# Optimization experiments

Measured on AMD Instinct MI355X. Metric: run time of the kernel, lower is better.

The kernel has to match this reference:

```python
import jax, jax.numpy as jnp
import numpy as np

B, S, D, H = 64, 128, 1024, 8
DK = D // H  # 128 == S, required by the module's (attn@V)@V quirk
DFF = 2048
EPS = 1e-12


def layernorm(x, w, b):
    u = x.mean(-1, keepdims=True)
    s = ((x - u) ** 2).mean(-1, keepdims=True)
    return w * (x - u) / jnp.sqrt(s + EPS) + b


def setup_inputs() -> dict:
    key = jax.random.key(0)
    ks = jax.random.split(key, 10)
    w = lambda k, shape: jax.random.normal(k, shape, jnp.float32) * 0.02
    return {
        "x": jax.random.normal(ks[0], (B, S, D), jnp.float32),
        "mask": jnp.ones((1, 1, S, S), jnp.int32),
        "Wq": w(ks[1], (D, D)), "bq": jnp.zeros((D,), jnp.float32),
        "Wk": w(ks[2], (D, D)), "bk": jnp.zeros((D,), jnp.float32),
        "Wv": w(ks[3], (D, D)), "bv": jnp.zeros((D,), jnp.float32),
        "Wo": w(ks[4], (D, D)), "bo": jnp.zeros((D,), jnp.float32),
        "ln1_w": jnp.ones((D,), jnp.float32), "ln1_b": jnp.zeros((D,), jnp.float32),
        "W1": w(ks[5], (DFF, D)), "b1": jnp.zeros((DFF,), jnp.float32),
        "W2": w(ks[6], (4 * D, DFF)), "b2": jnp.zeros((4 * D,), jnp.float32),
        "W3": w(ks[7], (D, 4 * D)), "b3": jnp.zeros((D,), jnp.float32),
        "ln2_w": jnp.ones((D,), jnp.float32), "ln2_b": jnp.zeros((D,), jnp.float32),
    }


def reference(x, mask, Wq, bq, Wk, bk, Wv, bv, Wo, bo, ln1_w, ln1_b,
              W1, b1, W2, b2, W3, b3, ln2_w, ln2_b):
    # QKV projections -> [B, H, S, DK]
    Q = (x @ Wq.T + bq).reshape(B, S, H, DK).transpose(0, 2, 1, 3)
    K = (x @ Wk.T + bk).reshape(B, S, H, DK).transpose(0, 2, 1, 3)
    V = (x @ Wv.T + bv).reshape(B, S, H, DK).transpose(0, 2, 1, 3)

    scores = jnp.einsum('bhqd,bhkd->bhqk', Q, K) / jnp.sqrt(jnp.float32(DK))
    scores = jnp.where(mask == 0, jnp.float32(-1e9), scores)
    attn = jax.nn.softmax(scores, axis=-1)  # dropout = identity (eval)
    av = jnp.matmul(attn, V)                 # [B,H,S,DK]
    # Faithful quirk in the source: multiply by V a second time (DK == S).
    ctx = jnp.matmul(av, V)                  # [B,H,S,DK]
    ctx = ctx.transpose(0, 2, 1, 3).reshape(B, S, D)
    attn_out = ctx @ Wo.T + bo

    h = layernorm(x + attn_out, ln1_w, ln1_b)

    f = jax.nn.relu(h @ W1.T + b1)           # [B,S,DFF]
    f = jax.nn.relu(f @ W2.T + b2)           # [B,S,4D]
    f = f @ W3.T + b3                        # [B,S,D]

    return layernorm(h + f, ln2_w, ln2_b)
```

## Files before the change

### kernel.cpp

```cpp
#include <hip/hip_runtime.h>
#include <hip/hip_bf16.h>

using bf16 = __hip_bfloat16;
typedef __attribute__((ext_vector_type(4))) float f32x4;
typedef __attribute__((ext_vector_type(8))) short bf16x8;

__device__ __forceinline__ unsigned short bfbits(float f) {
    bf16 h = __float2bfloat16(f);
    return __builtin_bit_cast(unsigned short, h);
}

__device__ __forceinline__ void g2l16(const void* g, void* l) {
    __builtin_amdgcn_global_load_lds(
        (const __attribute__((address_space(1))) unsigned int*)g,
        (__attribute__((address_space(3))) unsigned int*)l, 16, 0, 0);
}

__global__ void castk(const float* __restrict__ in, bf16* __restrict__ out, int n4) {
    int stride = gridDim.x * blockDim.x;
    for (int i = blockIdx.x * blockDim.x + threadIdx.x; i < n4; i += stride) {
        float4 v = reinterpret_cast<const float4*>(in)[i];
        ushort4 o;
        o.x = bfbits(v.x); o.y = bfbits(v.y); o.z = bfbits(v.z); o.w = bfbits(v.w);
        reinterpret_cast<ushort4*>(out)[i] = o;
    }
}

template<int EPI, int SPLITK>
__global__ __launch_bounds__(512, 2)
void gemm256(const bf16* __restrict__ A, const bf16* __restrict__ Bm,
             int N, int ldk, int kloop,
             const float* __restrict__ bias0, const float* __restrict__ bias1,
             const float* __restrict__ bias2,
             void* __restrict__ outp,
             bf16* __restrict__ q_o, bf16* __restrict__ k_o, bf16* __restrict__ v_o) {
    __shared__ __align__(16) char lds[98304];
    const int tid = threadIdx.x;
    const int lane = tid & 63, wave = tid >> 6;
    const int rlo = lane & 15, g = lane >> 4;
    const int wr = wave >> 2, wc = wave & 3;
    const int nbn = N >> 8;
    const int nwg = gridDim.x;
    int wg = (int)blockIdx.x;
    wg = (wg & 7) * (nwg >> 3) + (wg >> 3);
    int slice = 0;
    if constexpr (SPLITK) {
        int half = nwg >> 1;
        slice = (wg >= half) ? 1 : 0;
        wg -= slice * half;
    }
    const int bm = wg / nbn, bn = wg % nbn;
    const size_t ldb = (size_t)ldk * 2;
    const char* abase = (const char*)A + ((size_t)bm << 8) * ldb + (size_t)slice * kloop * 2;
    const char* bbase = (const char*)Bm + ((size_t)bn << 8) * ldb + (size_t)slice * kloop * 2;

    const int P = tid * 16;
    const int R = P >> 7;
    const int qs = (P & 127) ^ ((R & 7) << 4);
    const size_t goff0 = (size_t)(R * 2 + (qs >> 6)) * ldb + (qs & 63);
    const size_t ghalf = (size_t)128 * ldb;

    const int o_in = (((rlo & 1) << 6) | (g << 4)) ^ (((rlo >> 1) & 7) << 4);
    const int aoff = wr * 8192 + (rlo >> 1) * 128 + o_in;
    const int boff = 16384 + (wc >> 1) * 8192 + (wc & 1) * 4096 + (rlo >> 1) * 128 + o_in;

    const f32x4 fz = {0.f, 0.f, 0.f, 0.f};
    f32x4 acc[8][4];
#pragma unroll
    for (int i = 0; i < 8; ++i)
#pragma unroll
        for (int j = 0; j < 4; ++j) acc[i][j] = fz;

    auto stA = [&](int buf, int h, int kt) {
        g2l16(abase + goff0 + (size_t)h * ghalf + (size_t)kt * 64,
              lds + buf * 32768 + h * 8192 + P);
    };
    auto stB = [&](int buf, int h, int kt) {
        g2l16(bbase + goff0 + (size_t)h * ghalf + (size_t)kt * 64,
              lds + buf * 32768 + 16384 + h * 8192 + P);
    };

    stA(0, 0, 0); stA(0, 1, 0); stB(0, 0, 0); stB(0, 1, 0);
    stA(1, 0, 1); stA(1, 1, 1); stB(1, 0, 1); stB(1, 1, 1);
    asm volatile("s_waitcnt vmcnt(4)" ::: "memory");
    __builtin_amdgcn_s_barrier();
    __builtin_amdgcn_sched_barrier(0);

    const int NT = kloop >> 5;
    for (int kt = 0; kt < NT; ++kt) {
        const char* lb = lds + (kt % 3) * 32768;
        const int nbuf = (kt + 2) % 3;
        const bool pre = (kt + 2) < NT;

        bf16x8 bfr[4], afr[4];
#pragma unroll
        for (int nf = 0; nf < 4; ++nf)
            bfr[nf] = *reinterpret_cast<const bf16x8*>(lb + nf * 1024 + boff);
#pragma unroll
        for (int i = 0; i < 4; ++i)
            afr[i] = *reinterpret_cast<const bf16x8*>(lb + i * 1024 + aoff);
        if (pre) { stA(nbuf, 0, kt + 2); stA(nbuf, 1, kt + 2); }
        asm volatile("s_waitcnt lgkmcnt(0)");
        __builtin_amdgcn_s_setprio(1);
#pragma unroll
        for (int i = 0; i < 4; ++i)
#pragma unroll
            for (int nf = 0; nf < 4; ++nf)
                acc[i][nf] = __builtin_amdgcn_mfma_f32_16x16x32_bf16(afr[i], bfr[nf], acc[i][nf], 0, 0, 0);
        __builtin_amdgcn_s_setprio(0);

#pragma unroll
        for (int i = 0; i < 4; ++i)
            afr[i] = *reinterpret_cast<const bf16x8*>(lb + (4 + i) * 1024 + aoff);
        if (pre) { stB(nbuf, 0, kt + 2); stB(nbuf, 1, kt + 2); }
        asm volatile("s_waitcnt lgkmcnt(0)");
        __builtin_amdgcn_s_setprio(1);
#pragma unroll
        for (int i = 0; i < 4; ++i)
#pragma unroll
            for (int nf = 0; nf < 4; ++nf)
                acc[4 + i][nf] = __builtin_amdgcn_mfma_f32_16x16x32_bf16(afr[i], bfr[nf], acc[4 + i][nf], 0, 0, 0);
        __builtin_amdgcn_s_setprio(0);

        if (pre) {
            asm volatile("s_waitcnt vmcnt(4)" ::: "memory");
        } else if (kt + 1 < NT) {
            asm volatile("s_waitcnt vmcnt(0)" ::: "memory");
        }
        if (kt + 1 < NT) {
            __builtin_amdgcn_s_barrier();
            __builtin_amdgcn_sched_barrier(0);
        }
    }

    const int gm0 = (bm << 8) + wr * 128;
    const int gn0 = (bn << 8) + wc * 64;
#pragma unroll
    for (int mf = 0; mf < 8; ++mf) {
#pragma unroll
        for (int nf = 0; nf < 4; ++nf) {
            const int gnc = gn0 + nf * 16 + rlo;
#pragma unroll
            for (int r = 0; r < 4; ++r) {
                const int gmr = gm0 + mf * 16 + g * 4 + r;
                float val = acc[mf][nf][r];
                if constexpr (EPI == 0) {
                    int t = gnc >> 10;
                    const float* bp = (t == 0) ? bias0 : ((t == 1) ? bias1 : bias2);
                    val += bp[gnc & 1023];
                    bf16* dst = (t == 0) ? q_o : ((t == 1) ? k_o : v_o);
                    int hh = (gnc >> 7) & 7, d = gnc & 127;
                    int bb = gmr >> 7, s = gmr & 127;
                    dst[(((size_t)bb * 8 + hh) * 128 + s) * 128 + d] = __float2bfloat16(val);
                } else if constexpr (EPI == 1) {
                    val = fmaxf(val + bias0[gnc], 0.f);
                    ((bf16*)outp)[(size_t)gmr * N + gnc] = __float2bfloat16(val);
                } else {
                    float* pp = (float*)outp + (size_t)slice * 8388608;
                    pp[(size_t)gmr * N + gnc] = val;
                }
            }
        }
    }
}

template<int EPI>
__global__ __launch_bounds__(256, 2)
void gemm_bt(const bf16* __restrict__ A, const bf16* __restrict__ Bm,
             int M, int N, int K,
             const float* __restrict__ bias0, const float* __restrict__ resid,
             void* __restrict__ outp) {
    (void)M;
    __shared__ __align__(16) char As[8192];
    __shared__ __align__(16) char Bs[8192];
    int tid = threadIdx.x, wave = tid >> 6, lane = tid & 63;
    int nbn = N >> 7;
    int bm = blockIdx.x / nbn, bn = blockIdx.x % nbn;
    int wm = (wave >> 1) << 6, wn = (wave & 1) << 6;
    int rlo = lane & 15, g = lane >> 4;

    const char* abase = (const char*)(A + (size_t)(bm << 7) * K);
    const char* bbase = (const char*)(Bm + (size_t)(bn << 7) * K);

    const f32x4 fzero = {0.f, 0.f, 0.f, 0.f};
    f32x4 acc[4][4];
#pragma unroll
    for (int i = 0; i < 4; ++i)
#pragma unroll
        for (int j = 0; j < 4; ++j) acc[i][j] = fzero;

    int L0 = wave * 2048 + lane * 16;
    size_t ldbyte = (size_t)K * 2;

    for (int k0 = 0; k0 < K; k0 += 32) {
#pragma unroll
        for (int j = 0; j < 2; ++j) {
            int L = L0 + j * 1024;
            int row = L >> 6;
            int cb = (L & 63) ^ (((row >> 1) & 3) << 4);
            g2l16(abase + (size_t)row * ldbyte + (size_t)k0 * 2 + cb, As + wave * 2048 + j * 1024);
            g2l16(bbase + (size_t)row * ldbyte + (size_t)k0 * 2 + cb, Bs + wave * 2048 + j * 1024);
        }
        __syncthreads();
        bf16x8 af[4], bf8[4];
#pragma unroll
        for (int i = 0; i < 4; ++i) {
            int ra = wm + i * 16 + rlo;
            af[i] = *reinterpret_cast<const bf16x8*>(As + ra * 64 + ((g * 16) ^ (((ra >> 1) & 3) << 4)));
            int rb = wn + i * 16 + rlo;
            bf8[i] = *reinterpret_cast<const bf16x8*>(Bs + rb * 64 + ((g * 16) ^ (((rb >> 1) & 3) << 4)));
        }
#pragma unroll
        for (int mi = 0; mi < 4; ++mi)
#pragma unroll
            for (int ni = 0; ni < 4; ++ni)
                acc[mi][ni] = __builtin_amdgcn_mfma_f32_16x16x32_bf16(af[mi], bf8[ni], acc[mi][ni], 0, 0, 0);
        __syncthreads();
    }

    int gm0 = (bm << 7) + wm, gn0 = (bn << 7) + wn;
#pragma unroll
    for (int mi = 0; mi < 4; ++mi) {
#pragma unroll
        for (int ni = 0; ni < 4; ++ni) {
            int gnc = gn0 + ni * 16 + rlo;
#pragma unroll
            for (int r = 0; r < 4; ++r) {
                int gmr = gm0 + mi * 16 + g * 4 + r;
                float val = acc[mi][ni][r];
                val += bias0[gnc] + resid[(size_t)gmr * N + gnc];
                ((float*)outp)[(size_t)gmr * N + gnc] = val;
            }
        }
    }
}

__global__ __launch_bounds__(256)
void transpose_v(const bf16* __restrict__ V, bf16* __restrict__ VT) {
    __shared__ unsigned short t[128 * 132];
    int bh = blockIdx.x, tid = threadIdx.x;
    const unsigned short* src = (const unsigned short*)(V + (size_t)bh * 16384);
#pragma unroll
    for (int i = 0; i < 8; ++i) {
        int idx = tid + i * 256;
        int srow = idx >> 4;
        int c8 = (idx & 15) * 8;
        ushort4 a = reinterpret_cast<const ushort4*>(src + srow * 128 + c8)[0];
        ushort4 b = reinterpret_cast<const ushort4*>(src + srow * 128 + c8 + 4)[0];
        reinterpret_cast<ushort4*>(t + srow * 132 + c8)[0] = a;
        reinterpret_cast<ushort4*>(t + srow * 132 + c8 + 4)[0] = b;
    }
    __syncthreads();
    unsigned short* dst = (unsigned short*)(VT + (size_t)bh * 16384);
#pragma unroll
    for (int i = 0; i < 8; ++i) {
        int idx = tid + i * 256;
        int drow = idx >> 4;
        int s8 = (idx & 15) * 8;
        ushort4 a, b;
        a.x = t[(s8 + 0) * 132 + drow]; a.y = t[(s8 + 1) * 132 + drow];
        a.z = t[(s8 + 2) * 132 + drow]; a.w = t[(s8 + 3) * 132 + drow];
        b.x = t[(s8 + 4) * 132 + drow]; b.y = t[(s8 + 5) * 132 + drow];
        b.z = t[(s8 + 6) * 132 + drow]; b.w = t[(s8 + 7) * 132 + drow];
        reinterpret_cast<ushort4*>(dst + drow * 128 + s8)[0] = a;
        reinterpret_cast<ushort4*>(dst + drow * 128 + s8 + 4)[0] = b;
    }
}

__global__ __launch_bounds__(256, 2)
void attn_scores(const bf16* __restrict__ Q, const bf16* __restrict__ K, bf16* __restrict__ P) {
    __shared__ __align__(16) char Qs[32768];
    __shared__ __align__(16) char Ks[32768];
    int bh = blockIdx.x;
    int tid = threadIdx.x, wave = tid >> 6, lane = tid & 63;
    const char* qsrc = (const char*)(Q + (size_t)bh * 16384);
    const char* ksrc = (const char*)(K + (size_t)bh * 16384);
#pragma unroll
    for (int j = 0; j < 8; ++j) {
        int L = wave * 8192 + j * 1024 + lane * 16;
        int row = L >> 8;
        int cb = (L & 255) ^ ((row & 7) << 4);
        g2l16(qsrc + row * 256 + cb, Qs + wave * 8192 + j * 1024);
        g2l16(ksrc + row * 256 + cb, Ks + wave * 8192 + j * 1024);
    }
    __syncthreads();
    int rlo = lane & 15, g = lane >> 4;
    const f32x4 fzero = {0.f, 0.f, 0.f, 0.f};
    f32x4 acc[2][8];
#pragma unroll
    for (int mi = 0; mi < 2; ++mi)
#pragma unroll
        for (int ni = 0; ni < 8; ++ni) acc[mi][ni] = fzero;
#pragma unroll
    for (int kk = 0; kk < 4; ++kk) {
        bf16x8 aq[2], bk8[8];
#pragma unroll
        for (int mi = 0; mi < 2; ++mi) {
            int row = wave * 32 + mi * 16 + rlo;
            aq[mi] = *reinterpret_cast<const bf16x8*>(Qs + row * 256 + ((kk * 64 + g * 16) ^ ((row & 7) << 4)));
        }
#pragma unroll
        for (int ni = 0; ni < 8; ++ni) {
            int row = ni * 16 + rlo;
            bk8[ni] = *reinterpret_cast<const bf16x8*>(Ks + row * 256 + ((kk * 64 + g * 16) ^ ((row & 7) << 4)));
        }
#pragma unroll
        for (int mi = 0; mi < 2; ++mi)
#pragma unroll
            for (int ni = 0; ni < 8; ++ni)
                acc[mi][ni] = __builtin_amdgcn_mfma_f32_16x16x32_bf16(aq[mi], bk8[ni], acc[mi][ni], 0, 0, 0);
    }
    const float scale = 0.088388347648318447f;
    unsigned short* pdst = (unsigned short*)(P + (size_t)bh * 16384);
#pragma unroll
    for (int mi = 0; mi < 2; ++mi) {
#pragma unroll
        for (int r = 0; r < 4; ++r) {
            float m = -3e38f;
#pragma unroll
            for (int ni = 0; ni < 8; ++ni) m = fmaxf(m, acc[mi][ni][r]);
#pragma unroll
            for (int o = 1; o < 16; o <<= 1) m = fmaxf(m, __shfl_xor(m, o));
            m *= scale;
            float e[8];
            float sum = 0.f;
#pragma unroll
            for (int ni = 0; ni < 8; ++ni) { e[ni] = __expf(acc[mi][ni][r] * scale - m); sum += e[ni]; }
#pragma unroll
            for (int o = 1; o < 16; o <<= 1) sum += __shfl_xor(sum, o);
            float inv = 1.f / sum;
            int qrow = wave * 32 + mi * 16 + g * 4 + r;
#pragma unroll
            for (int ni = 0; ni < 8; ++ni)
                pdst[qrow * 128 + ni * 16 + rlo] = bfbits(e[ni] * inv);
        }
    }
}

__global__ __launch_bounds__(256, 2)
void attn_ctx(const bf16* __restrict__ P, const bf16* __restrict__ VT, bf16* __restrict__ CTX) {
    __shared__ __align__(16) char Vs[32768];
    __shared__ __align__(16) char Ts[32768];
    int bh = blockIdx.x, b = bh >> 3, h = bh & 7;
    int tid = threadIdx.x, wave = tid >> 6, lane = tid & 63;
    const char* vsrc = (const char*)(VT + (size_t)bh * 16384);
#pragma unroll
    for (int j = 0; j < 8; ++j) {
        int L = wave * 8192 + j * 1024 + lane * 16;
        int row = L >> 8;
        int cb = (L & 255) ^ ((row & 7) << 4);
        g2l16(vsrc + row * 256 + cb, Vs + wave * 8192 + j * 1024);
    }
    __syncthreads();
    int rlo = lane & 15, g = lane >> 4;
    const char* psrc = (const char*)(P + (size_t)bh * 16384);
    const f32x4 fzero = {0.f, 0.f, 0.f, 0.f};
    f32x4 accT[2][8];
#pragma unroll
    for (int mi = 0; mi < 2; ++mi)
#pragma unroll
        for (int ni = 0; ni < 8; ++ni) accT[mi][ni] = fzero;
#pragma unroll
    for (int kk = 0; kk < 4; ++kk) {
        bf16x8 ap[2], bv8[8];
#pragma unroll
        for (int mi = 0; mi < 2; ++mi) {
            int row = wave * 32 + mi * 16 + rlo;
            ap[mi] = *reinterpret_cast<const bf16x8*>(psrc + (size_t)row * 256 + kk * 64 + g * 16);
        }
#pragma unroll
        for (int ni = 0; ni < 8; ++ni) {
            int row = ni * 16 + rlo;
            bv8[ni] = *reinterpret_cast<const bf16x8*>(Vs + row * 256 + ((kk * 64 + g * 16) ^ ((row & 7) << 4)));
        }
#pragma unroll
        for (int mi = 0; mi < 2; ++mi)
#pragma unroll
            for (int ni = 0; ni < 8; ++ni)
                accT[mi][ni] = __builtin_amdgcn_mfma_f32_16x16x32_bf16(ap[mi], bv8[ni], accT[mi][ni], 0, 0, 0);
    }
#pragma unroll
    for (int mi = 0; mi < 2; ++mi)
#pragma unroll
        for (int ni = 0; ni < 8; ++ni)
#pragma unroll
            for (int r = 0; r < 4; ++r) {
                int trow = wave * 32 + mi * 16 + g * 4 + r;
                int cbyte = ((ni * 16 + rlo) * 2) ^ ((trow & 7) << 4);
                *(unsigned short*)(Ts + trow * 256 + cbyte) = bfbits(accT[mi][ni][r]);
            }
    __syncthreads();
    f32x4 accC[2][8];
#pragma unroll
    for (int mi = 0; mi < 2; ++mi)
#pragma unroll
        for (int ni = 0; ni < 8; ++ni) accC[mi][ni] = fzero;
#pragma unroll
    for (int kk = 0; kk < 4; ++kk) {
        bf16x8 at[2], bv8[8];
#pragma unroll
        for (int mi = 0; mi < 2; ++mi) {
            int row = wave * 32 + mi * 16 + rlo;
            at[mi] = *reinterpret_cast<const bf16x8*>(Ts + row * 256 + ((kk * 64 + g * 16) ^ ((row & 7) << 4)));
        }
#pragma unroll
        for (int ni = 0; ni < 8; ++ni) {
            int row = ni * 16 + rlo;
            bv8[ni] = *reinterpret_cast<const bf16x8*>(Vs + row * 256 + ((kk * 64 + g * 16) ^ ((row & 7) << 4)));
        }
#pragma unroll
        for (int mi = 0; mi < 2; ++mi)
#pragma unroll
            for (int ni = 0; ni < 8; ++ni)
                accC[mi][ni] = __builtin_amdgcn_mfma_f32_16x16x32_bf16(at[mi], bv8[ni], accC[mi][ni], 0, 0, 0);
    }
    unsigned short* cdst = (unsigned short*)CTX;
#pragma unroll
    for (int mi = 0; mi < 2; ++mi)
#pragma unroll
        for (int ni = 0; ni < 8; ++ni)
#pragma unroll
            for (int r = 0; r < 4; ++r) {
                int q = wave * 32 + mi * 16 + g * 4 + r;
                int gm = b * 128 + q;
                int col = h * 128 + ni * 16 + rlo;
                cdst[(size_t)gm * 1024 + col] = bfbits(accC[mi][ni][r]);
            }
}

template<int MODE>
__global__ __launch_bounds__(256)
void ln_k(const float* __restrict__ Y, const float* __restrict__ w, const float* __restrict__ b,
          float* __restrict__ Hf, bf16* __restrict__ Hb) {
    int row = blockIdx.x, tid = threadIdx.x;
    float4 v = reinterpret_cast<const float4*>(Y + (size_t)row * 1024)[tid];
    float s = v.x + v.y + v.z + v.w;
    float q = v.x * v.x + v.y * v.y + v.z * v.z + v.w * v.w;
#pragma unroll
    for (int o = 1; o < 64; o <<= 1) { s += __shfl_xor(s, o); q += __shfl_xor(q, o); }
    __shared__ float ss[4], sq[4];
    if ((tid & 63) == 0) { ss[tid >> 6] = s; sq[tid >> 6] = q; }
    __syncthreads();
    s = ss[0] + ss[1] + ss[2] + ss[3];
    q = sq[0] + sq[1] + sq[2] + sq[3];
    float u = s * (1.f / 1024.f);
    float var = fmaxf(q * (1.f / 1024.f) - u * u, 0.f);
    float rstd = rsqrtf(var + 1e-12f);
    float4 wv = reinterpret_cast<const float4*>(w)[tid];
    float4 bv = reinterpret_cast<const float4*>(b)[tid];
    float o0 = wv.x * (v.x - u) * rstd + bv.x;
    float o1 = wv.y * (v.y - u) * rstd + bv.y;
    float o2 = wv.z * (v.z - u) * rstd + bv.z;
    float o3 = wv.w * (v.w - u) * rstd + bv.w;
    reinterpret_cast<float4*>(Hf + (size_t)row * 1024)[tid] = make_float4(o0, o1, o2, o3);
    if constexpr (MODE == 0) {
        ushort4 ob;
        ob.x = bfbits(o0); ob.y = bfbits(o1); ob.z = bfbits(o2); ob.w = bfbits(o3);
        reinterpret_cast<ushort4*>(Hb)[row * 256 + tid] = ob;
    }
}

__global__ __launch_bounds__(256)
void ln2k(const float* __restrict__ PA, const float* __restrict__ PB,
          const float* __restrict__ b3, const float* __restrict__ resid,
          const float* __restrict__ w, const float* __restrict__ b,
          float* __restrict__ out) {
    int row = blockIdx.x, tid = threadIdx.x;
    size_t off = (size_t)row * 256 + tid;
    float4 pa = reinterpret_cast<const float4*>(PA)[off];
    float4 pb = reinterpret_cast<const float4*>(PB)[off];
    float4 bi = reinterpret_cast<const float4*>(b3)[tid];
    float4 rs = reinterpret_cast<const float4*>(resid)[off];
    float4 v = make_float4(pa.x + pb.x + bi.x + rs.x, pa.y + pb.y + bi.y + rs.y,
                           pa.z + pb.z + bi.z + rs.z, pa.w + pb.w + bi.w + rs.w);
    float s = v.x + v.y + v.z + v.w;
    float q = v.x * v.x + v.y * v.y + v.z * v.z + v.w * v.w;
#pragma unroll
    for (int o = 1; o < 64; o <<= 1) { s += __shfl_xor(s, o); q += __shfl_xor(q, o); }
    __shared__ float ss[4], sq[4];
    if ((tid & 63) == 0) { ss[tid >> 6] = s; sq[tid >> 6] = q; }
    __syncthreads();
    s = ss[0] + ss[1] + ss[2] + ss[3];
    q = sq[0] + sq[1] + sq[2] + sq[3];
    float u = s * (1.f / 1024.f);
    float var = fmaxf(q * (1.f / 1024.f) - u * u, 0.f);
    float rstd = rsqrtf(var + 1e-12f);
    float4 wv = reinterpret_cast<const float4*>(w)[tid];
    float4 bv = reinterpret_cast<const float4*>(b)[tid];
    float4 o4;
    o4.x = wv.x * (v.x - u) * rstd + bv.x;
    o4.y = wv.y * (v.y - u) * rstd + bv.y;
    o4.z = wv.z * (v.z - u) * rstd + bv.z;
    o4.w = wv.w * (v.w - u) * rstd + bv.w;
    reinterpret_cast<float4*>(out)[off] = o4;
}

extern "C" void kernel_launch(void* const* d_in, const int* in_sizes, int n_in,
                              void* d_out, int out_size, void* d_ws, size_t ws_size,
                              hipStream_t stream) {
    (void)in_sizes; (void)n_in; (void)out_size; (void)ws_size;
    const float* x    = (const float*)d_in[0];
    const float* Wq   = (const float*)d_in[2];
    const float* bq   = (const float*)d_in[3];
    const float* Wk   = (const float*)d_in[4];
    const float* bk   = (const float*)d_in[5];
    const float* Wv   = (const float*)d_in[6];
    const float* bv   = (const float*)d_in[7];
    const float* Wo   = (const float*)d_in[8];
    const float* bo   = (const float*)d_in[9];
    const float* ln1w = (const float*)d_in[10];
    const float* ln1b = (const float*)d_in[11];
    const float* W1   = (const float*)d_in[12];
    const float* b1   = (const float*)d_in[13];
    const float* W2   = (const float*)d_in[14];
    const float* b2   = (const float*)d_in[15];
    const float* W3   = (const float*)d_in[16];
    const float* b3   = (const float*)d_in[17];
    const float* ln2w = (const float*)d_in[18];
    const float* ln2b = (const float*)d_in[19];

    char* ws = (char*)d_ws;
    bf16*  XB    = (bf16*)(ws + 0);
    bf16*  WQKVB = (bf16*)(ws + 16777216);
    bf16*  WOB   = (bf16*)(ws + 23068672);
    bf16*  W1B   = (bf16*)(ws + 25165824);
    bf16*  W2B   = (bf16*)(ws + 29360128);
    bf16*  W3B   = (bf16*)(ws + 46137344);
    bf16*  Qb    = (bf16*)(ws + 54525952);
    bf16*  Kb    = (bf16*)(ws + 71303168);
    bf16*  Vb    = (bf16*)(ws + 88080384);
    bf16*  VTb   = (bf16*)(ws + 104857600);
    bf16*  Pb    = (bf16*)(ws + 121634816);
    bf16*  CTX   = (bf16*)(ws + 138412032);
    float* Y2    = (float*)(ws + 155189248);
    float* H32   = (float*)(ws + 188743680);
    bf16*  HB    = (bf16*)(ws + 222298112);
    bf16*  F1    = (bf16*)(ws + 155189248);
    bf16*  F2    = (bf16*)(ws + 54525952);
    float* PW3   = (float*)(ws + 121634816);
    float* PW3b  = (float*)(ws + 0);

    auto cast = [&](const float* s, bf16* dd, int n4) {
        int nb = (n4 + 255) / 256; if (nb > 2048) nb = 2048;
        castk<<<nb, 256, 0, stream>>>(s, dd, n4);
    };
    cast(x,  XB,             2097152);
    cast(Wq, WQKVB,           262144);
    cast(Wk, WQKVB + 1048576, 262144);
    cast(Wv, WQKVB + 2097152, 262144);
    cast(Wo, WOB,             262144);
    cast(W1, W1B,             524288);
    cast(W2, W2B,            2097152);
    cast(W3, W3B,            1048576);

    gemm256<0, 0><<<384, 512, 0, stream>>>(XB, WQKVB, 3072, 1024, 1024,
                                           bq, bk, bv, nullptr, Qb, Kb, Vb);
    transpose_v<<<512, 256, 0, stream>>>(Vb, VTb);
    attn_scores<<<512, 256, 0, stream>>>(Qb, Kb, Pb);
    attn_ctx<<<512, 256, 0, stream>>>(Pb, VTb, CTX);
    gemm_bt<2><<<512, 256, 0, stream>>>(CTX, WOB, 8192, 1024, 1024, bo, x, (void*)Y2);
    ln_k<0><<<8192, 256, 0, stream>>>(Y2, ln1w, ln1b, H32, HB);
    gemm256<1, 0><<<256, 512, 0, stream>>>(HB, W1B, 2048, 1024, 1024,
                                           b1, nullptr, nullptr, (void*)F1, nullptr, nullptr, nullptr);
    gemm256<1, 0><<<512, 512, 0, stream>>>(F1, W2B, 4096, 2048, 2048,
                                           b2, nullptr, nullptr, (void*)F2, nullptr, nullptr, nullptr);
    gemm256<2, 1><<<256, 512, 0, stream>>>(F2, W3B, 1024, 4096, 2048,
                                           nullptr, nullptr, nullptr, (void*)PW3, nullptr, nullptr, nullptr);
    (void)PW3b;
    ln2k<<<8192, 256, 0, stream>>>(PW3, PW3 + 8388608, b3, H32, ln2w, ln2b, (float*)d_out);
}
```

Baseline: 437.4 us.

## Fuse attention kernels, write V transposed from QKV GEMM, batch casts

Merges attn_scores and attn_ctx into one kernel that keeps the softmax probabilities in LDS (reusing the Q buffer) instead of writing P to global memory and reading it back. The QKV GEMM epilogue now writes V directly in transposed layout, which removes the separate transpose kernel. The eight cast launches are folded into one kernel that does a per-element branch lookup across a contiguous workspace. The fused attention kernel uses 96KB of LDS with launch bounds of 1, which may lower occupancy, and the transposed V store is strided and may coalesce poorly.

```diff
diff --git a/kernel.cpp b/kernel.cpp
--- a/kernel.cpp
+++ b/kernel.cpp
@@ -16,13 +16,27 @@
         (__attribute__((address_space(3))) unsigned int*)l, 16, 0, 0);
 }
 
-__global__ void castk(const float* __restrict__ in, bf16* __restrict__ out, int n4) {
+struct CastArgs {
+    const float* src[8];
+    int end[8];
+};
+__global__ __launch_bounds__(256)
+void castall(CastArgs a, ushort4* __restrict__ out) {
     int stride = gridDim.x * blockDim.x;
-    for (int i = blockIdx.x * blockDim.x + threadIdx.x; i < n4; i += stride) {
-        float4 v = reinterpret_cast<const float4*>(in)[i];
+    for (int i = blockIdx.x * blockDim.x + threadIdx.x; i < 6815744; i += stride) {
+        const float* sp; int beg;
+        if      (i < a.end[0]) { sp = a.src[0]; beg = 0; }
+        else if (i < a.end[1]) { sp = a.src[1]; beg = a.end[0]; }
+        else if (i < a.end[2]) { sp = a.src[2]; beg = a.end[1]; }
+        else if (i < a.end[3]) { sp = a.src[3]; beg = a.end[2]; }
+        else if (i < a.end[4]) { sp = a.src[4]; beg = a.end[3]; }
+        else if (i < a.end[5]) { sp = a.src[5]; beg = a.end[4]; }
+        else if (i < a.end[6]) { sp = a.src[6]; beg = a.end[5]; }
+        else                   { sp = a.src[7]; beg = a.end[6]; }
+        float4 v = reinterpret_cast<const float4*>(sp)[i - beg];
         ushort4 o;
         o.x = bfbits(v.x); o.y = bfbits(v.y); o.z = bfbits(v.z); o.w = bfbits(v.w);
-        reinterpret_cast<ushort4*>(out)[i] = o;
+        out[i] = o;
     }
 }
 
@@ -151,7 +165,10 @@
                     bf16* dst = (t == 0) ? q_o : ((t == 1) ? k_o : v_o);
                     int hh = (gnc >> 7) & 7, d = gnc & 127;
                     int bb = gmr >> 7, s = gmr & 127;
-                    dst[(((size_t)bb * 8 + hh) * 128 + s) * 128 + d] = __float2bfloat16(val);
+                    size_t idx = (t == 2)
+                        ? ((((size_t)bb * 8 + hh) * 128 + d) * 128 + s)
+                        : ((((size_t)bb * 8 + hh) * 128 + s) * 128 + d);
+                    dst[idx] = __float2bfloat16(val);
                 } else if constexpr (EPI == 1) {
                     val = fmaxf(val + bias0[gnc], 0.f);
                     ((bf16*)outp)[(size_t)gmr * N + gnc] = __float2bfloat16(val);
@@ -235,46 +252,17 @@
     }
 }
 
-__global__ __launch_bounds__(256)
-void transpose_v(const bf16* __restrict__ V, bf16* __restrict__ VT) {
-    __shared__ unsigned short t[128 * 132];
-    int bh = blockIdx.x, tid = threadIdx.x;
-    const unsigned short* src = (const unsigned short*)(V + (size_t)bh * 16384);
-#pragma unroll
-    for (int i = 0; i < 8; ++i) {
-        int idx = tid + i * 256;
-        int srow = idx >> 4;
-        int c8 = (idx & 15) * 8;
-        ushort4 a = reinterpret_cast<const ushort4*>(src + srow * 128 + c8)[0];
-        ushort4 b = reinterpret_cast<const ushort4*>(src + srow * 128 + c8 + 4)[0];
-        reinterpret_cast<ushort4*>(t + srow * 132 + c8)[0] = a;
-        reinterpret_cast<ushort4*>(t + srow * 132 + c8 + 4)[0] = b;
-    }
-    __syncthreads();
-    unsigned short* dst = (unsigned short*)(VT + (size_t)bh * 16384);
-#pragma unroll
-    for (int i = 0; i < 8; ++i) {
-        int idx = tid + i * 256;
-        int drow = idx >> 4;
-        int s8 = (idx & 15) * 8;
-        ushort4 a, b;
-        a.x = t[(s8 + 0) * 132 + drow]; a.y = t[(s8 + 1) * 132 + drow];
-        a.z = t[(s8 + 2) * 132 + drow]; a.w = t[(s8 + 3) * 132 + drow];
-        b.x = t[(s8 + 4) * 132 + drow]; b.y = t[(s8 + 5) * 132 + drow];
-        b.z = t[(s8 + 6) * 132 + drow]; b.w = t[(s8 + 7) * 132 + drow];
-        reinterpret_cast<ushort4*>(dst + drow * 128 + s8)[0] = a;
-        reinterpret_cast<ushort4*>(dst + drow * 128 + s8 + 4)[0] = b;
-    }
-}
-
-__global__ __launch_bounds__(256, 2)
-void attn_scores(const bf16* __restrict__ Q, const bf16* __restrict__ K, bf16* __restrict__ P) {
+__global__ __launch_bounds__(256, 1)
+void attn_fused(const bf16* __restrict__ Q, const bf16* __restrict__ K,
+                const bf16* __restrict__ VT, bf16* __restrict__ CTX) {
     __shared__ __align__(16) char Qs[32768];
     __shared__ __align__(16) char Ks[32768];
-    int bh = blockIdx.x;
+    __shared__ __align__(16) char Vs[32768];
+    int bh = blockIdx.x, b = bh >> 3, h = bh & 7;
     int tid = threadIdx.x, wave = tid >> 6, lane = tid & 63;
     const char* qsrc = (const char*)(Q + (size_t)bh * 16384);
     const char* ksrc = (const char*)(K + (size_t)bh * 16384);
+    const char* vsrc = (const char*)(VT + (size_t)bh * 16384);
 #pragma unroll
     for (int j = 0; j < 8; ++j) {
         int L = wave * 8192 + j * 1024 + lane * 16;
@@ -282,10 +270,12 @@
         int cb = (L & 255) ^ ((row & 7) << 4);
         g2l16(qsrc + row * 256 + cb, Qs + wave * 8192 + j * 1024);
         g2l16(ksrc + row * 256 + cb, Ks + wave * 8192 + j * 1024);
+        g2l16(vsrc + row * 256 + cb, Vs + wave * 8192 + j * 1024);
     }
     __syncthreads();
     int rlo = lane & 15, g = lane >> 4;
     const f32x4 fzero = {0.f, 0.f, 0.f, 0.f};
+
     f32x4 acc[2][8];
 #pragma unroll
     for (int mi = 0; mi < 2; ++mi)
@@ -310,8 +300,8 @@
             for (int ni = 0; ni < 8; ++ni)
                 acc[mi][ni] = __builtin_amdgcn_mfma_f32_16x16x32_bf16(aq[mi], bk8[ni], acc[mi][ni], 0, 0, 0);
     }
+
     const float scale = 0.088388347648318447f;
-    unsigned short* pdst = (unsigned short*)(P + (size_t)bh * 16384);
 #pragma unroll
     for (int mi = 0; mi < 2; ++mi) {
 #pragma unroll
@@ -331,30 +321,14 @@
             float inv = 1.f / sum;
             int qrow = wave * 32 + mi * 16 + g * 4 + r;
 #pragma unroll
-            for (int ni = 0; ni < 8; ++ni)
-                pdst[qrow * 128 + ni * 16 + rlo] = bfbits(e[ni] * inv);
-        }
-    }
-}
-
-__global__ __launch_bounds__(256, 2)
-void attn_ctx(const bf16* __restrict__ P, const bf16* __restrict__ VT, bf16* __restrict__ CTX) {
-    __shared__ __align__(16) char Vs[32768];
-    __shared__ __align__(16) char Ts[32768];
-    int bh = blockIdx.x, b = bh >> 3, h = bh & 7;
-    int tid = threadIdx.x, wave = tid >> 6, lane = tid & 63;
-    const char* vsrc = (const char*)(VT + (size_t)bh * 16384);
-#pragma unroll
-    for (int j = 0; j < 8; ++j) {
-        int L = wave * 8192 + j * 1024 + lane * 16;
-        int row = L >> 8;
-        int cb = (L & 255) ^ ((row & 7) << 4);
-        g2l16(vsrc + row * 256 + cb, Vs + wave * 8192 + j * 1024);
+            for (int ni = 0; ni < 8; ++ni) {
+                int cbyte = ((ni * 16 + rlo) * 2) ^ ((qrow & 7) << 4);
+                *(unsigned short*)(Qs + qrow * 256 + cbyte) = bfbits(e[ni] * inv);
+            }
+        }
     }
     __syncthreads();
-    int rlo = lane & 15, g = lane >> 4;
-    const char* psrc = (const char*)(P + (size_t)bh * 16384);
-    const f32x4 fzero = {0.f, 0.f, 0.f, 0.f};
+
     f32x4 accT[2][8];
 #pragma unroll
     for (int mi = 0; mi < 2; ++mi)
@@ -366,7 +340,7 @@
 #pragma unroll
         for (int mi = 0; mi < 2; ++mi) {
             int row = wave * 32 + mi * 16 + rlo;
-            ap[mi] = *reinterpret_cast<const bf16x8*>(psrc + (size_t)row * 256 + kk * 64 + g * 16);
+            ap[mi] = *reinterpret_cast<const bf16x8*>(Qs + row * 256 + ((kk * 64 + g * 16) ^ ((row & 7) << 4)));
         }
 #pragma unroll
         for (int ni = 0; ni < 8; ++ni) {
@@ -387,9 +361,10 @@
             for (int r = 0; r < 4; ++r) {
                 int trow = wave * 32 + mi * 16 + g * 4 + r;
                 int cbyte = ((ni * 16 + rlo) * 2) ^ ((trow & 7) << 4);
-                *(unsigned short*)(Ts + trow * 256 + cbyte) = bfbits(accT[mi][ni][r]);
+                *(unsigned short*)(Ks + trow * 256 + cbyte) = bfbits(accT[mi][ni][r]);
             }
     __syncthreads();
+
     f32x4 accC[2][8];
 #pragma unroll
     for (int mi = 0; mi < 2; ++mi)
@@ -401,7 +376,7 @@
 #pragma unroll
         for (int mi = 0; mi < 2; ++mi) {
             int row = wave * 32 + mi * 16 + rlo;
-            at[mi] = *reinterpret_cast<const bf16x8*>(Ts + row * 256 + ((kk * 64 + g * 16) ^ ((row & 7) << 4)));
+            at[mi] = *reinterpret_cast<const bf16x8*>(Ks + row * 256 + ((kk * 64 + g * 16) ^ ((row & 7) << 4)));
         }
 #pragma unroll
         for (int ni = 0; ni < 8; ++ni) {
@@ -528,9 +503,7 @@
     bf16*  W3B   = (bf16*)(ws + 46137344);
     bf16*  Qb    = (bf16*)(ws + 54525952);
     bf16*  Kb    = (bf16*)(ws + 71303168);
-    bf16*  Vb    = (bf16*)(ws + 88080384);
-    bf16*  VTb   = (bf16*)(ws + 104857600);
-    bf16*  Pb    = (bf16*)(ws + 121634816);
+    bf16*  VTb   = (bf16*)(ws + 88080384);
     bf16*  CTX   = (bf16*)(ws + 138412032);
     float* Y2    = (float*)(ws + 155189248);
     float* H32   = (float*)(ws + 188743680);
@@ -538,26 +511,17 @@
     bf16*  F1    = (bf16*)(ws + 155189248);
     bf16*  F2    = (bf16*)(ws + 54525952);
     float* PW3   = (float*)(ws + 121634816);
-    float* PW3b  = (float*)(ws + 0);
-
-    auto cast = [&](const float* s, bf16* dd, int n4) {
-        int nb = (n4 + 255) / 256; if (nb > 2048) nb = 2048;
-        castk<<<nb, 256, 0, stream>>>(s, dd, n4);
-    };
-    cast(x,  XB,             2097152);
-    cast(Wq, WQKVB,           262144);
-    cast(Wk, WQKVB + 1048576, 262144);
-    cast(Wv, WQKVB + 2097152, 262144);
-    cast(Wo, WOB,             262144);
-    cast(W1, W1B,             524288);
-    cast(W2, W2B,            2097152);
-    cast(W3, W3B,            1048576);
+
+    CastArgs ca;
+    ca.src[0] = x;  ca.src[1] = Wq; ca.src[2] = Wk; ca.src[3] = Wv;
+    ca.src[4] = Wo; ca.src[5] = W1; ca.src[6] = W2; ca.src[7] = W3;
+    ca.end[0] = 2097152; ca.end[1] = 2359296; ca.end[2] = 2621440; ca.end[3] = 2883584;
+    ca.end[4] = 3145728; ca.end[5] = 3670016; ca.end[6] = 5767168; ca.end[7] = 6815744;
+    castall<<<2048, 256, 0, stream>>>(ca, (ushort4*)ws);
 
     gemm256<0, 0><<<384, 512, 0, stream>>>(XB, WQKVB, 3072, 1024, 1024,
-                                           bq, bk, bv, nullptr, Qb, Kb, Vb);
-    transpose_v<<<512, 256, 0, stream>>>(Vb, VTb);
-    attn_scores<<<512, 256, 0, stream>>>(Qb, Kb, Pb);
-    attn_ctx<<<512, 256, 0, stream>>>(Pb, VTb, CTX);
+                                           bq, bk, bv, nullptr, Qb, Kb, VTb);
+    attn_fused<<<512, 256, 0, stream>>>(Qb, Kb, VTb, CTX);
     gemm_bt<2><<<512, 256, 0, stream>>>(CTX, WOB, 8192, 1024, 1024, bo, x, (void*)Y2);
     ln_k<0><<<8192, 256, 0, stream>>>(Y2, ln1w, ln1b, H32, HB);
     gemm256<1, 0><<<256, 512, 0, stream>>>(HB, W1B, 2048, 1024, 1024,
@@ -566,6 +530,5 @@
                                            b2, nullptr, nullptr, (void*)F2, nullptr, nullptr, nullptr);
     gemm256<2, 1><<<256, 512, 0, stream>>>(F2, W3B, 1024, 4096, 2048,
                                            nullptr, nullptr, nullptr, (void*)PW3, nullptr, nullptr, nullptr);
-    (void)PW3b;
     ln2k<<<8192, 256, 0, stream>>>(PW3, PW3 + 8388608, b3, H32, ln2w, ln2b, (float*)d_out);
 }
```

Result: no change. 438.8 us (+0.3%).
